# Kernel tuning notes

Hardware: AMD Instinct MI355X
Metric: run time of the kernel (lower is better)

Reference implementation:

```python
import jax, jax.numpy as jnp
import numpy as np

B, S, D = 128, 512, 1024          # batch, ctx seqlen, model dim
GEN_V, INP_V, OUT_V = 50000, 30000, 50257  # gen vocab, input vocab, output vocab


def setup_inputs() -> dict:
    key = jax.random.key(0)
    ks = jax.random.split(key, 7)
    x = jax.random.normal(ks[0], (B, D), jnp.float32)
    alphas = jax.random.uniform(ks[1], (B, S), jnp.float32)
    alphas = alphas / alphas.sum(-1, keepdims=True)  # normalized attention probs
    ctx_inp = jax.random.randint(ks[2], (B, S), 0, INP_V)
    gen_to_out = jax.random.randint(ks[3], (GEN_V,), 0, OUT_V)
    inp_to_out = jax.random.randint(ks[4], (INP_V,), 0, OUT_V)
    W_gate = jax.random.normal(ks[5], (D, 1), jnp.float32) * 0.02
    b_gate = jnp.zeros((1,), jnp.float32)
    W_gen = jax.random.normal(ks[6], (D, GEN_V), jnp.float32) * 0.02
    b_gen = jnp.zeros((GEN_V,), jnp.float32)
    return {"x": x, "alphas": alphas, "W_gate": W_gate, "b_gate": b_gate,
            "W_gen": W_gen, "b_gen": b_gen, "ctx_inp": ctx_inp,
            "gen_to_out": gen_to_out, "inp_to_out": inp_to_out}


def reference(x, alphas, W_gate, b_gate, W_gen, b_gen, ctx_inp, gen_to_out, inp_to_out):
    # gate: probability of generating vs pointing  [B,1]
    interp = jax.nn.sigmoid(x @ W_gate + b_gate)
    # generation distribution over gen vocab       [B,GEN_V]
    gen_probs = jax.nn.softmax(x @ W_gen + b_gen, axis=-1)
    # scatter_add gen probs into output vocab (same index map for all rows)
    out_gen = jax.ops.segment_sum(gen_probs.T, gen_to_out, num_segments=OUT_V).T  # [B,OUT_V]
    # scatter_add pointer probs into output vocab (per-row indices)
    ctx_out = inp_to_out[ctx_inp]  # [B,S]
    rows = jnp.arange(x.shape[0])[:, None]
    out_ptr = jnp.zeros((x.shape[0], OUT_V), x.dtype).at[rows, ctx_out].add(alphas)
    # interpolated mixture
    return interp * out_gen + (1.0 - interp) * out_ptr
```

## Files before the change

### kernel.cpp

```cpp
#include <hip/hip_runtime.h>
#include <hip/hip_bf16.h>
#include <cstdint>
#include <cstddef>

#define B_ 128
#define D_ 1024
#define GEN_V_ 50000
#define OUT_V_ 50257
#define S_ 512

#define NTILE 64
#define NBLK 782
#define BK 64
#define LD 72
#define CAP 8

typedef __attribute__((ext_vector_type(8))) short bf16x8;
typedef __attribute__((ext_vector_type(8))) unsigned short u16x8;
typedef __attribute__((ext_vector_type(4))) float f32x4;

__device__ __forceinline__ unsigned short f2bf(float f) {
  unsigned u = __float_as_uint(f);
  u += 0x7fffu + ((u >> 16) & 1u);
  return (unsigned short)(u >> 16);
}

__global__ __launch_bounds__(512, 4) void gemm_kernel(
    const float* __restrict__ x, const float* __restrict__ W,
    const float* __restrict__ bgen, float* __restrict__ elog,
    float* __restrict__ rowpart) {
  __shared__ unsigned short sA[B_][LD];
  __shared__ unsigned short sB[NTILE][LD];
  __shared__ float srow[B_];
  int tid = threadIdx.x;
  int lane = tid & 63;
  int wv = tid >> 6;
  int wm = wv & 1;
  int wn = wv >> 1;
  int nbase = blockIdx.x * NTILE;
  int l15 = lane & 15;
  int quad = lane >> 4;
  int koff0 = quad * 8;

  f32x4 acc[4];
#pragma unroll
  for (int i = 0; i < 4; i++) acc[i] = (f32x4){0.f, 0.f, 0.f, 0.f};

  int bn = lane;
  int kc = wv;
  bool colv = (nbase + bn) < GEN_V_;
  const float* Wcol = W + (size_t)kc * 8 * GEN_V_ + nbase + bn;

  const float4* xg = (const float4*)x;

  for (int k0 = 0; k0 < D_; k0 += BK) {
    int kb4 = k0 >> 2;
#pragma unroll
    for (int i = 0; i < 4; i++) {
      int q = tid + i * 512;
      int m = q >> 4, c4 = q & 15;
      float4 v = xg[(size_t)m * (D_ / 4) + kb4 + c4];
      ushort4 h;
      h.x = f2bf(v.x); h.y = f2bf(v.y); h.z = f2bf(v.z); h.w = f2bf(v.w);
      *(ushort4*)&sA[m][c4 * 4] = h;
    }
    {
      const float* Wp = Wcol + (size_t)k0 * GEN_V_;
      u16x8 hh;
#pragma unroll
      for (int j = 0; j < 8; j++) {
        float w = colv ? Wp[(size_t)j * GEN_V_] : 0.f;
        hh[j] = f2bf(w);
      }
      *(u16x8*)&sB[bn][kc * 8] = hh;
    }
    __syncthreads();
#pragma unroll
    for (int ks = 0; ks < BK; ks += 32) {
      int koff = ks + koff0;
      bf16x8 bfr = *(const bf16x8*)&sB[wn * 16 + l15][koff];
      bf16x8 af[4];
#pragma unroll
      for (int mt = 0; mt < 4; mt++)
        af[mt] = *(const bf16x8*)&sA[wm * 64 + mt * 16 + l15][koff];
#pragma unroll
      for (int mt = 0; mt < 4; mt++)
        acc[mt] = __builtin_amdgcn_mfma_f32_16x16x32_bf16(af[mt], bfr, acc[mt], 0, 0, 0);
    }
    __syncthreads();
  }

  if (tid < B_) srow[tid] = 0.f;
  __syncthreads();
  int cg = nbase + wn * 16 + l15;
  bool cv = cg < GEN_V_;
  float bgv = cv ? bgen[cg] : 0.f;
  int rquad = quad * 4;
#pragma unroll
  for (int mt = 0; mt < 4; mt++) {
    int rb = wm * 64 + mt * 16 + rquad;
#pragma unroll
    for (int r = 0; r < 4; r++) {
      float e = __expf(acc[mt][r] + bgv);
      float contrib = cv ? e : 0.f;
      if (cv) elog[(size_t)(rb + r) * GEN_V_ + cg] = e;
#pragma unroll
      for (int o = 1; o < 16; o <<= 1) contrib += __shfl_xor(contrib, o);
      if (l15 == 0) atomicAdd(&srow[rb + r], contrib);
    }
  }
  __syncthreads();
  if (tid < B_) rowpart[(size_t)tid * NBLK + blockIdx.x] = srow[tid];
}

__global__ void build_index_kernel(const int* __restrict__ g2o, int* __restrict__ cnt,
                                   int* __restrict__ vlist, int* __restrict__ novf,
                                   int* __restrict__ ovf) {
  int v = blockIdx.x * 256 + threadIdx.x;
  if (v < GEN_V_) {
    int o = g2o[v];
    int slot = atomicAdd(&cnt[o], 1);
    if (slot < CAP) {
      vlist[o * CAP + slot] = v;
    } else {
      int i = atomicAdd(novf, 1);
      ovf[2 * i] = o;
      ovf[2 * i + 1] = v;
    }
  }
}

__global__ void rowsum_gate_kernel(const float* __restrict__ rowpart,
                                   const float* __restrict__ x, const float* __restrict__ Wg,
                                   const float* __restrict__ bg,
                                   float* __restrict__ interp, float* __restrict__ rowscale) {
  int b = blockIdx.x, t = threadIdx.x;
  const float* rp = rowpart + (size_t)b * NBLK;
  float s = 0.f;
  for (int i = t; i < NBLK; i += 256) s += rp[i];
  const float4* xr = (const float4*)(x + (size_t)b * D_);
  const float4* wr = (const float4*)Wg;
  float4 xv = xr[t], wv = wr[t];
  float g = xv.x * wv.x + xv.y * wv.y + xv.z * wv.z + xv.w * wv.w;
  for (int o = 32; o > 0; o >>= 1) {
    s += __shfl_down(s, o);
    g += __shfl_down(g, o);
  }
  __shared__ float reds[4], redg[4];
  int lane = t & 63, w = t >> 6;
  if (lane == 0) { reds[w] = s; redg[w] = g; }
  __syncthreads();
  if (t == 0) {
    float tot = redg[0] + redg[1] + redg[2] + redg[3] + bg[0];
    float itp = 1.f / (1.f + __expf(-tot));
    float sum = reds[0] + reds[1] + reds[2] + reds[3];
    interp[b] = itp;
    rowscale[b] = itp / sum;
  }
}

__global__ void gather_gen_kernel(const float* __restrict__ elog, const int* __restrict__ cnt,
                                  const int* __restrict__ vlist,
                                  const float* __restrict__ rowscale, float* __restrict__ out) {
  int o = blockIdx.x * 256 + threadIdx.x;
  int b = blockIdx.y;
  if (o < OUT_V_) {
    int c = cnt[o];
    if (c > CAP) c = CAP;
    const float* lrow = elog + (size_t)b * GEN_V_;
    const int* vl = vlist + (size_t)o * CAP;
    float s = 0.f;
    for (int j = 0; j < c; j++) s += lrow[vl[j]];
    out[(size_t)b * OUT_V_ + o] = s * rowscale[b];
  }
}

__global__ void ovf_kernel(const int* __restrict__ novf, const int* __restrict__ ovf,
                           const float* __restrict__ elog, const float* __restrict__ rowscale,
                           float* __restrict__ out) {
  int n = novf[0];
  if (n == 0) return;
  int total = n * B_;
  for (int i = blockIdx.x * 256 + threadIdx.x; i < total; i += gridDim.x * 256) {
    int e = i >> 7;
    int b = i & 127;
    int o = ovf[2 * e];
    int v = ovf[2 * e + 1];
    atomicAdd(&out[(size_t)b * OUT_V_ + o], rowscale[b] * elog[(size_t)b * GEN_V_ + v]);
  }
}

__global__ void scatter_ptr_kernel(const float* __restrict__ alphas, const int* __restrict__ ctx,
                                   const int* __restrict__ i2o, const float* __restrict__ interp,
                                   float* __restrict__ out) {
  int b = blockIdx.x, s = threadIdx.x;
  float w = 1.f - interp[b];
  int o = i2o[ctx[b * S_ + s]];
  atomicAdd(&out[(size_t)b * OUT_V_ + o], w * alphas[b * S_ + s]);
}

extern "C" void kernel_launch(void* const* d_in, const int* in_sizes, int n_in,
                              void* d_out, int out_size, void* d_ws, size_t ws_size,
                              hipStream_t stream) {
  const float* x      = (const float*)d_in[0];
  const float* alphas = (const float*)d_in[1];
  const float* Wg     = (const float*)d_in[2];
  const float* bg     = (const float*)d_in[3];
  const float* Wgen   = (const float*)d_in[4];
  const float* bgen   = (const float*)d_in[5];
  const int*   ctx    = (const int*)d_in[6];
  const int*   g2o    = (const int*)d_in[7];
  const int*   i2o    = (const int*)d_in[8];
  float* out = (float*)d_out;

  float* elog      = (float*)d_ws;
  float* interp    = elog + (size_t)B_ * GEN_V_;
  float* rowscale  = interp + B_;
  float* rowpart   = rowscale + B_;
  int*   cnt       = (int*)(rowpart + (size_t)B_ * NBLK);
  int*   novf      = cnt + OUT_V_;
  int*   vlist     = novf + 1;
  int*   ovf       = vlist + (size_t)OUT_V_ * CAP;

  hipMemsetAsync(cnt, 0, (OUT_V_ + 1) * sizeof(int), stream);

  build_index_kernel<<<(GEN_V_ + 255) / 256, 256, 0, stream>>>(g2o, cnt, vlist, novf, ovf);
  gemm_kernel<<<NBLK, 512, 0, stream>>>(x, Wgen, bgen, elog, rowpart);
  rowsum_gate_kernel<<<B_, 256, 0, stream>>>(rowpart, x, Wg, bg, interp, rowscale);
  gather_gen_kernel<<<dim3((OUT_V_ + 255) / 256, B_), 256, 0, stream>>>(
      elog, cnt, vlist, rowscale, out);
  ovf_kernel<<<64, 256, 0, stream>>>(novf, ovf, elog, rowscale, out);
  scatter_ptr_kernel<<<B_, S_, 0, stream>>>(alphas, ctx, i2o, interp, out);
}
```

Before: 406.6 us.

## Double GEMM N-tile to 128 and remap gather blocks for row locality

The GEMM kernel now computes 128 output columns per block instead of 64. Each wave holds two N subtiles, so every A fragment loaded from LDS feeds two MFMAs and the x-to-bf16 conversion is amortized over twice as many columns. The gather kernel switches to a 1D grid in which consecutive blocks cover different batch rows for the same output column range, which is meant to improve cache reuse of the cnt/vlist index reads. The trade-off is more accumulator registers per thread and half as many GEMM blocks, 391 on a device with 256 CUs, which risks load imbalance in the last wave.

```diff
diff --git a/kernel.cpp b/kernel.cpp
--- a/kernel.cpp
+++ b/kernel.cpp
@@ -9,8 +9,8 @@
 #define OUT_V_ 50257
 #define S_ 512
 
-#define NTILE 64
-#define NBLK 782
+#define NTILE 128
+#define NBLK 391
 #define BK 64
 #define LD 72
 #define CAP 8
@@ -42,14 +42,16 @@
   int quad = lane >> 4;
   int koff0 = quad * 8;
 
-  f32x4 acc[4];
-#pragma unroll
-  for (int i = 0; i < 4; i++) acc[i] = (f32x4){0.f, 0.f, 0.f, 0.f};
-
-  int bn = lane;
-  int kc = wv;
+  f32x4 acc[4][2];
+#pragma unroll
+  for (int i = 0; i < 4; i++)
+#pragma unroll
+    for (int j = 0; j < 2; j++) acc[i][j] = (f32x4){0.f, 0.f, 0.f, 0.f};
+
+  int bn = tid & 127;
+  int kc = tid >> 7;
   bool colv = (nbase + bn) < GEN_V_;
-  const float* Wcol = W + (size_t)kc * 8 * GEN_V_ + nbase + bn;
+  const float* Wcol = W + (size_t)kc * 16 * GEN_V_ + nbase + bn;
 
   const float4* xg = (const float4*)x;
 
@@ -66,47 +68,60 @@
     }
     {
       const float* Wp = Wcol + (size_t)k0 * GEN_V_;
-      u16x8 hh;
+      u16x8 h0, h1;
 #pragma unroll
       for (int j = 0; j < 8; j++) {
         float w = colv ? Wp[(size_t)j * GEN_V_] : 0.f;
-        hh[j] = f2bf(w);
-      }
-      *(u16x8*)&sB[bn][kc * 8] = hh;
+        h0[j] = f2bf(w);
+      }
+#pragma unroll
+      for (int j = 0; j < 8; j++) {
+        float w = colv ? Wp[(size_t)(j + 8) * GEN_V_] : 0.f;
+        h1[j] = f2bf(w);
+      }
+      *(u16x8*)&sB[bn][kc * 16] = h0;
+      *(u16x8*)&sB[bn][kc * 16 + 8] = h1;
     }
     __syncthreads();
 #pragma unroll
     for (int ks = 0; ks < BK; ks += 32) {
       int koff = ks + koff0;
-      bf16x8 bfr = *(const bf16x8*)&sB[wn * 16 + l15][koff];
+      bf16x8 bfr[2];
+      bfr[0] = *(const bf16x8*)&sB[wn * 32 + l15][koff];
+      bfr[1] = *(const bf16x8*)&sB[wn * 32 + 16 + l15][koff];
       bf16x8 af[4];
 #pragma unroll
       for (int mt = 0; mt < 4; mt++)
         af[mt] = *(const bf16x8*)&sA[wm * 64 + mt * 16 + l15][koff];
 #pragma unroll
-      for (int mt = 0; mt < 4; mt++)
-        acc[mt] = __builtin_amdgcn_mfma_f32_16x16x32_bf16(af[mt], bfr, acc[mt], 0, 0, 0);
+      for (int mt = 0; mt < 4; mt++) {
+        acc[mt][0] = __builtin_amdgcn_mfma_f32_16x16x32_bf16(af[mt], bfr[0], acc[mt][0], 0, 0, 0);
+        acc[mt][1] = __builtin_amdgcn_mfma_f32_16x16x32_bf16(af[mt], bfr[1], acc[mt][1], 0, 0, 0);
+      }
     }
     __syncthreads();
   }
 
   if (tid < B_) srow[tid] = 0.f;
   __syncthreads();
-  int cg = nbase + wn * 16 + l15;
-  bool cv = cg < GEN_V_;
-  float bgv = cv ? bgen[cg] : 0.f;
   int rquad = quad * 4;
 #pragma unroll
-  for (int mt = 0; mt < 4; mt++) {
-    int rb = wm * 64 + mt * 16 + rquad;
-#pragma unroll
-    for (int r = 0; r < 4; r++) {
-      float e = __expf(acc[mt][r] + bgv);
-      float contrib = cv ? e : 0.f;
-      if (cv) elog[(size_t)(rb + r) * GEN_V_ + cg] = e;
-#pragma unroll
-      for (int o = 1; o < 16; o <<= 1) contrib += __shfl_xor(contrib, o);
-      if (l15 == 0) atomicAdd(&srow[rb + r], contrib);
+  for (int nt = 0; nt < 2; nt++) {
+    int cg = nbase + wn * 32 + nt * 16 + l15;
+    bool cv = cg < GEN_V_;
+    float bgv = cv ? bgen[cg] : 0.f;
+#pragma unroll
+    for (int mt = 0; mt < 4; mt++) {
+      int rb = wm * 64 + mt * 16 + rquad;
+#pragma unroll
+      for (int r = 0; r < 4; r++) {
+        float e = __expf(acc[mt][nt][r] + bgv);
+        float contrib = cv ? e : 0.f;
+        if (cv) elog[(size_t)(rb + r) * GEN_V_ + cg] = e;
+#pragma unroll
+        for (int o = 1; o < 16; o <<= 1) contrib += __shfl_xor(contrib, o);
+        if (l15 == 0) atomicAdd(&srow[rb + r], contrib);
+      }
     }
   }
   __syncthreads();
@@ -159,11 +174,13 @@
   }
 }
 
+#define GATHER_NB (128 * 197)
 __global__ void gather_gen_kernel(const float* __restrict__ elog, const int* __restrict__ cnt,
                                   const int* __restrict__ vlist,
                                   const float* __restrict__ rowscale, float* __restrict__ out) {
-  int o = blockIdx.x * 256 + threadIdx.x;
-  int b = blockIdx.y;
+  int id = blockIdx.x;
+  int b = (id & 7) * 16 + ((id >> 3) & 15);
+  int o = (id >> 7) * 256 + threadIdx.x;
   if (o < OUT_V_) {
     int c = cnt[o];
     if (c > CAP) c = CAP;
@@ -227,8 +244,7 @@
   build_index_kernel<<<(GEN_V_ + 255) / 256, 256, 0, stream>>>(g2o, cnt, vlist, novf, ovf);
   gemm_kernel<<<NBLK, 512, 0, stream>>>(x, Wgen, bgen, elog, rowpart);
   rowsum_gate_kernel<<<B_, 256, 0, stream>>>(rowpart, x, Wg, bg, interp, rowscale);
-  gather_gen_kernel<<<dim3((OUT_V_ + 255) / 256, B_), 256, 0, stream>>>(
-      elog, cnt, vlist, rowscale, out);
+  gather_gen_kernel<<<GATHER_NB, 256, 0, stream>>>(elog, cnt, vlist, rowscale, out);
   ovf_kernel<<<64, 256, 0, stream>>>(novf, ovf, elog, rowscale, out);
   scatter_ptr_kernel<<<B_, S_, 0, stream>>>(alphas, ctx, i2o, interp, out);
 }
```

After: 397.7 us. 1.02x faster.
